# Kernel optimization log

Hardware: AMD Instinct MI355X
Metric: run time of the kernel (lower is better)

The kernel has to match this reference:

```python
import jax, jax.numpy as jnp
import numpy as np

# Config matching init_kwargs: layer_nb=1 -> stride 16, image 608x608 -> 38x38 grid
B, CIN, H, W = 32, 512, 38, 38
NA, NC = 3, 80
STRIDE = 16.0
ANCHORS = np.array([[30.0, 61.0], [62.0, 45.0], [59.0, 119.0]], dtype=np.float32)


def setup_inputs() -> dict:
    key = jax.random.key(0)
    k1, k2, k3 = jax.random.split(key, 3)
    xin = jax.random.normal(k1, (B, CIN, H, W), dtype=jnp.float32)
    # 1x1 conv weight stored as (out_ch, in_ch); out_ch = NA*(NC+5) = 255
    conv_w = jax.random.normal(k2, (NA * (NC + 5), CIN), dtype=jnp.float32) * 0.02
    conv_b = jax.random.normal(k3, (NA * (NC + 5),), dtype=jnp.float32) * 0.01
    return {"xin": xin, "conv_w": conv_w, "conv_b": conv_b}


def reference(xin, conv_w, conv_b):
    # 1x1 conv == channel GEMM; fuse the NCHW->NHWC permute into the einsum
    fm = jnp.einsum('bchw,oc->bhwo', xin, conv_w) + conv_b  # [B,H,W,255]
    fm = fm.reshape(B, H, W, NA, NC + 5)
    tx, ty, tw, th = fm[..., 0], fm[..., 1], fm[..., 2], fm[..., 3]
    # grid offsets (precomputed via broadcasting instead of per-call numpy rebuild)
    x_off = jnp.arange(W, dtype=fm.dtype)[None, None, :, None]   # broadcast over B,H,NA
    y_off = jnp.arange(H, dtype=fm.dtype)[None, :, None, None]   # broadcast over B,W,NA
    anchors = jnp.asarray(ANCHORS, dtype=fm.dtype)               # [NA,2]
    bx = (jax.nn.sigmoid(tx) + x_off) * STRIDE
    by = (jax.nn.sigmoid(ty) + y_off) * STRIDE
    bw = jnp.exp(tw) * anchors[:, 0]
    bh = jnp.exp(th) * anchors[:, 1]
    boxes = jnp.stack([bx, by, bw, bh], axis=-1)                 # [B,H,W,NA,4]
    # concat decoded boxes with raw objectness + class logits -> [B,H,W,NA,85]
    return jnp.concatenate([boxes, fm[..., 4:]], axis=-1)
```

## Files before the change

kernel.cpp:

```cpp
#include <hip/hip_runtime.h>
#include <hip/hip_bf16.h>
#include <cstdint>
#include <cstddef>

#define CIN_K  512
#define WW_    38
#define BHW    1444
#define NOUT   255
#define MTOT   46208

#define BM     32
#define ROW_E  520
#define EP_DW  260

typedef __attribute__((ext_vector_type(8))) short  bf16x8;
typedef __attribute__((ext_vector_type(4))) float  floatx4;

static __device__ __forceinline__ unsigned f2bf(float f) {
    unsigned u = __builtin_bit_cast(unsigned, f);
    return (u + 0x7FFFu + ((u >> 16) & 1u)) >> 16;
}

static __device__ __forceinline__ unsigned pk2bf(float a, float b) {
    __hip_bfloat162 h = __float22bfloat162_rn(make_float2(a, b));
    unsigned r;
    __builtin_memcpy(&r, &h, 4);
    return r;
}

__global__ void conv_w_to_bf16(const float* __restrict__ cw,
                               unsigned short* __restrict__ wb) {
    int tg   = blockIdx.x * 256 + threadIdx.x;
    int base = tg * 8;
    int n    = base >> 9;
    unsigned rr[4] = {0u, 0u, 0u, 0u};
    if (n < NOUT) {
        float4 v0 = *(const float4*)(cw + base);
        float4 v1 = *(const float4*)(cw + base + 4);
        rr[0] = f2bf(v0.x) | (f2bf(v0.y) << 16);
        rr[1] = f2bf(v0.z) | (f2bf(v0.w) << 16);
        rr[2] = f2bf(v1.x) | (f2bf(v1.y) << 16);
        rr[3] = f2bf(v1.z) | (f2bf(v1.w) << 16);
    }
    *(uint4*)(wb + base) = *(uint4*)rr;
}

__global__ __launch_bounds__(256, 4)
void yolo_head(const float* __restrict__ xin,
               const unsigned short* __restrict__ wb,
               const float* __restrict__ cb,
               float* __restrict__ out)
{
    __shared__ unsigned smem[BM * (ROW_E / 2)];
    unsigned short* As = (unsigned short*)smem;

    const int t    = threadIdx.x;
    const int w    = t >> 6;
    const int lane = t & 63;
    const int l15  = lane & 15;
    const int q    = lane >> 4;

    const int orig = blockIdx.x;
    const int xcd  = orig & 7;
    const int rank = orig >> 3;
    const int wgid = (xcd < 4 ? xcd * 181 : 724 + (xcd - 4) * 180) + rank;
    const int m0   = wgid * BM;

    const int mq4 = (t & 7) * 4;
    const int kq4 = (t >> 3) * 4;
    const int m4  = m0 + mq4;
    const int bi  = m4 / BHW;
    const int hw  = m4 - bi * BHW;
    const float* pb0 = xin + (size_t)bi * (CIN_K * BHW) + hw;

    alignas(16) float vv[4][4][4];
#pragma unroll
    for (int it = 0; it < 4; ++it)
#pragma unroll
        for (int kk = 0; kk < 4; ++kk)
            *(float4*)&vv[it][kk][0] =
                *(const float4*)(pb0 + (size_t)(it * 128 + kq4 + kk) * BHW);
#pragma unroll
    for (int it = 0; it < 4; ++it)
#pragma unroll
        for (int r = 0; r < 4; ++r) {
            unsigned lo = pk2bf(vv[it][0][r], vv[it][1][r]);
            unsigned hi = pk2bf(vv[it][2][r], vv[it][3][r]);
            *(uint2*)(&As[(mq4 + r) * ROW_E + it * 128 + kq4]) = make_uint2(lo, hi);
        }

    floatx4 acc[2][4];
#pragma unroll
    for (int i = 0; i < 2; ++i)
#pragma unroll
        for (int j = 0; j < 4; ++j)
            acc[i][j] = (floatx4){0.f, 0.f, 0.f, 0.f};

    const unsigned short* pbw = wb + (size_t)(w * 64 + l15) * CIN_K + q * 8;

    __syncthreads();

#pragma unroll
    for (int kc = 0; kc < 16; ++kc) {
        bf16x8 bfr[4], af[2];
#pragma unroll
        for (int j = 0; j < 4; ++j) {
            uint4 bv = *(const uint4*)(pbw + (size_t)j * 16 * CIN_K + kc * 32);
            bfr[j] = __builtin_bit_cast(bf16x8, bv);
        }
#pragma unroll
        for (int i = 0; i < 2; ++i) {
            int4 av = *(const int4*)(&As[(i * 16 + l15) * ROW_E + kc * 32 + q * 8]);
            af[i] = __builtin_bit_cast(bf16x8, av);
        }
#pragma unroll
        for (int i = 0; i < 2; ++i)
#pragma unroll
            for (int j = 0; j < 4; ++j)
                acc[i][j] = __builtin_amdgcn_mfma_f32_16x16x32_bf16(
                                af[i], bfr[j], acc[i][j], 0, 0, 0);
    }

#pragma unroll
    for (int j = 0; j < 4; ++j) {
        int   n    = w * 64 + j * 16 + l15;
        int   nc   = n < NOUT ? n : NOUT - 1;
        int   ai   = nc / 85;
        int   ji   = nc - ai * 85;
        float bias = cb[nc];
        float aw   = (ai == 0) ? 30.f : (ai == 1) ? 62.f : 59.f;
        float ah   = (ai == 0) ? 61.f : (ai == 1) ? 45.f : 119.f;
#pragma unroll
        for (int i = 0; i < 2; ++i)
#pragma unroll
            for (int r = 0; r < 4; ++r) {
                int   md  = m0 + i * 16 + q * 4 + r;
                int   rem = md % BHW;
                int   hh  = rem / WW_;
                float v   = acc[i][j][r] + bias;
                float res;
                if (ji == 0)      res = (1.f / (1.f + __expf(-v)) + (float)(rem - hh * WW_)) * 16.f;
                else if (ji == 1) res = (1.f / (1.f + __expf(-v)) + (float)hh) * 16.f;
                else if (ji == 2) res = __expf(v) * aw;
                else if (ji == 3) res = __expf(v) * ah;
                else              res = v;
                acc[i][j][r] = res;
            }
    }

    __syncthreads();
    float* EP = (float*)smem;
#pragma unroll
    for (int i = 0; i < 2; ++i)
#pragma unroll
        for (int j = 0; j < 4; ++j)
#pragma unroll
            for (int r = 0; r < 4; ++r)
                EP[(i * 16 + q * 4 + r) * EP_DW + w * 64 + j * 16 + l15] =
                    acc[i][j][r];
    __syncthreads();

    {
        const float* EPb = (const float*)smem + (w * 8) * EP_DW;
        float*       ob  = out + (size_t)(m0 + w * 8) * NOUT;
#pragma unroll
        for (int s2 = 0; s2 < 8; ++s2) {
            int f4 = s2 * 64 + lane;
            if (f4 < 510) {
                int   f = f4 * 4;
                float vs[4];
#pragma unroll
                for (int e = 0; e < 4; ++e) {
                    int fe = f + e;
                    int mr = fe / NOUT;
                    int x  = fe - mr * NOUT;
                    vs[e]  = EPb[mr * EP_DW + x];
                }
                *(float4*)(ob + f) = make_float4(vs[0], vs[1], vs[2], vs[3]);
            }
        }
    }
}

extern "C" void kernel_launch(void* const* d_in, const int* in_sizes, int n_in,
                              void* d_out, int out_size, void* d_ws, size_t ws_size,
                              hipStream_t stream) {
    const float* xin = (const float*)d_in[0];
    const float* cw  = (const float*)d_in[1];
    const float* cb  = (const float*)d_in[2];
    float*       out = (float*)d_out;
    unsigned short* wb = (unsigned short*)d_ws;

    hipLaunchKernelGGL(conv_w_to_bf16, dim3(64), dim3(256), 0, stream, cw, wb);
    hipLaunchKernelGGL(yolo_head, dim3(MTOT / BM), dim3(256), 0, stream,
                       xin, wb, cb, out);
}
```

Baseline: 196.6 us.

## Load activations directly into MFMA fragments and double the M tile

Removes the LDS staging of the activation tile. Each lane now gathers its 8 K-values straight from global memory, strided by BHW, and converts them to bf16 inside the K loop. BM goes from 32 to 64 so each weight fragment load feeds twice as many MFMAs, with the grid remapping and the epilogue adjusted to two 32-row passes. The cost is scalar, strided, 4-byte global loads on the critical path instead of float4 loads, more accumulator registers, and lower occupancy.

```diff
diff --git a/kernel.cpp b/kernel.cpp
--- a/kernel.cpp
+++ b/kernel.cpp
@@ -9,8 +9,7 @@
 #define NOUT   255
 #define MTOT   46208
 
-#define BM     32
-#define ROW_E  520
+#define BM     64
 #define EP_DW  260
 
 typedef __attribute__((ext_vector_type(8))) short  bf16x8;
@@ -45,14 +44,13 @@
     *(uint4*)(wb + base) = *(uint4*)rr;
 }
 
-__global__ __launch_bounds__(256, 4)
+__global__ __launch_bounds__(256, 3)
 void yolo_head(const float* __restrict__ xin,
                const unsigned short* __restrict__ wb,
                const float* __restrict__ cb,
                float* __restrict__ out)
 {
-    __shared__ unsigned smem[BM * (ROW_E / 2)];
-    unsigned short* As = (unsigned short*)smem;
+    __shared__ unsigned smem[32 * EP_DW];
 
     const int t    = threadIdx.x;
     const int w    = t >> 6;
@@ -63,58 +61,49 @@
     const int orig = blockIdx.x;
     const int xcd  = orig & 7;
     const int rank = orig >> 3;
-    const int wgid = (xcd < 4 ? xcd * 181 : 724 + (xcd - 4) * 180) + rank;
+    const int wgid = (xcd < 2 ? xcd * 91 : 182 + (xcd - 2) * 90) + rank;
     const int m0   = wgid * BM;
 
-    const int mq4 = (t & 7) * 4;
-    const int kq4 = (t >> 3) * 4;
-    const int m4  = m0 + mq4;
-    const int bi  = m4 / BHW;
-    const int hw  = m4 - bi * BHW;
-    const float* pb0 = xin + (size_t)bi * (CIN_K * BHW) + hw;
+    const float* pa[4];
+#pragma unroll
+    for (int i = 0; i < 4; ++i) {
+        int m  = m0 + i * 16 + l15;
+        int bi = m / BHW;
+        int hw = m - bi * BHW;
+        pa[i] = xin + (size_t)bi * (CIN_K * BHW) + hw + (size_t)(q * 8) * BHW;
+    }
 
-    alignas(16) float vv[4][4][4];
+    floatx4 acc[4][4];
 #pragma unroll
-    for (int it = 0; it < 4; ++it)
-#pragma unroll
-        for (int kk = 0; kk < 4; ++kk)
-            *(float4*)&vv[it][kk][0] =
-                *(const float4*)(pb0 + (size_t)(it * 128 + kq4 + kk) * BHW);
-#pragma unroll
-    for (int it = 0; it < 4; ++it)
-#pragma unroll
-        for (int r = 0; r < 4; ++r) {
-            unsigned lo = pk2bf(vv[it][0][r], vv[it][1][r]);
-            unsigned hi = pk2bf(vv[it][2][r], vv[it][3][r]);
-            *(uint2*)(&As[(mq4 + r) * ROW_E + it * 128 + kq4]) = make_uint2(lo, hi);
-        }
-
-    floatx4 acc[2][4];
-#pragma unroll
-    for (int i = 0; i < 2; ++i)
+    for (int i = 0; i < 4; ++i)
 #pragma unroll
         for (int j = 0; j < 4; ++j)
             acc[i][j] = (floatx4){0.f, 0.f, 0.f, 0.f};
 
     const unsigned short* pbw = wb + (size_t)(w * 64 + l15) * CIN_K + q * 8;
 
-    __syncthreads();
-
 #pragma unroll
     for (int kc = 0; kc < 16; ++kc) {
-        bf16x8 bfr[4], af[2];
+        bf16x8 bfr[4], af[4];
 #pragma unroll
         for (int j = 0; j < 4; ++j) {
             uint4 bv = *(const uint4*)(pbw + (size_t)j * 16 * CIN_K + kc * 32);
             bfr[j] = __builtin_bit_cast(bf16x8, bv);
         }
 #pragma unroll
-        for (int i = 0; i < 2; ++i) {
-            int4 av = *(const int4*)(&As[(i * 16 + l15) * ROW_E + kc * 32 + q * 8]);
-            af[i] = __builtin_bit_cast(bf16x8, av);
+        for (int i = 0; i < 4; ++i) {
+            float a8[8];
+#pragma unroll
+            for (int u = 0; u < 8; ++u)
+                a8[u] = pa[i][(size_t)(kc * 32 + u) * BHW];
+            unsigned d[4];
+#pragma unroll
+            for (int e = 0; e < 4; ++e)
+                d[e] = pk2bf(a8[2 * e], a8[2 * e + 1]);
+            af[i] = __builtin_bit_cast(bf16x8, *(uint4*)d);
         }
 #pragma unroll
-        for (int i = 0; i < 2; ++i)
+        for (int i = 0; i < 4; ++i)
 #pragma unroll
             for (int j = 0; j < 4; ++j)
                 acc[i][j] = __builtin_amdgcn_mfma_f32_16x16x32_bf16(
@@ -131,7 +120,7 @@
         float aw   = (ai == 0) ? 30.f : (ai == 1) ? 62.f : 59.f;
         float ah   = (ai == 0) ? 61.f : (ai == 1) ? 45.f : 119.f;
 #pragma unroll
-        for (int i = 0; i < 2; ++i)
+        for (int i = 0; i < 4; ++i)
 #pragma unroll
             for (int r = 0; r < 4; ++r) {
                 int   md  = m0 + i * 16 + q * 4 + r;
@@ -148,21 +137,24 @@
             }
     }
 
-    __syncthreads();
     float* EP = (float*)smem;
 #pragma unroll
-    for (int i = 0; i < 2; ++i)
+    for (int p = 0; p < 2; ++p) {
+        __syncthreads();
 #pragma unroll
-        for (int j = 0; j < 4; ++j)
+        for (int i2 = 0; i2 < 2; ++i2) {
+            const int i = p * 2 + i2;
 #pragma unroll
-            for (int r = 0; r < 4; ++r)
-                EP[(i * 16 + q * 4 + r) * EP_DW + w * 64 + j * 16 + l15] =
-                    acc[i][j][r];
-    __syncthreads();
+            for (int j = 0; j < 4; ++j)
+#pragma unroll
+                for (int r = 0; r < 4; ++r)
+                    EP[(i2 * 16 + q * 4 + r) * EP_DW + w * 64 + j * 16 + l15] =
+                        acc[i][j][r];
+        }
+        __syncthreads();
 
-    {
         const float* EPb = (const float*)smem + (w * 8) * EP_DW;
-        float*       ob  = out + (size_t)(m0 + w * 8) * NOUT;
+        float*       ob  = out + (size_t)(m0 + p * 32 + w * 8) * NOUT;
 #pragma unroll
         for (int s2 = 0; s2 < 8; ++s2) {
             int f4 = s2 * 64 + lane;
```

Result: slower. 210.8 us (+7.2%).

## Double M tile to 64 rows with 8 waves and K-chunked LDS staging

Applied to the files above, without the earlier changes.

Raises the block tile from 32 to 64 output rows with 512 threads arranged as 2x4 waves, so each weight fragment fetched from global memory is reused across twice as many rows. The A tile is staged through LDS in two K halves of 256, which keeps shared memory the same size but adds an extra barrier and reload step. The epilogue writes out the two 32-row halves in turn through the shared buffer. The risk is lower occupancy from the larger blocks and less overlap, since the load of the second K half waits behind the barrier.

```diff
diff --git a/kernel.cpp b/kernel.cpp
--- a/kernel.cpp
+++ b/kernel.cpp
@@ -9,8 +9,9 @@
 #define NOUT   255
 #define MTOT   46208
 
-#define BM     32
-#define ROW_E  520
+#define BM     64
+#define KCH    256
+#define ROW_E  260
 #define EP_DW  260
 
 typedef __attribute__((ext_vector_type(8))) short  bf16x8;
@@ -45,7 +46,7 @@
     *(uint4*)(wb + base) = *(uint4*)rr;
 }
 
-__global__ __launch_bounds__(256, 4)
+__global__ __launch_bounds__(512, 6)
 void yolo_head(const float* __restrict__ xin,
                const unsigned short* __restrict__ wb,
                const float* __restrict__ cb,
@@ -55,7 +56,9 @@
     unsigned short* As = (unsigned short*)smem;
 
     const int t    = threadIdx.x;
-    const int w    = t >> 6;
+    const int wv   = t >> 6;
+    const int wm   = wv >> 2;
+    const int wn   = wv & 3;
     const int lane = t & 63;
     const int l15  = lane & 15;
     const int q    = lane >> 4;
@@ -63,32 +66,16 @@
     const int orig = blockIdx.x;
     const int xcd  = orig & 7;
     const int rank = orig >> 3;
-    const int wgid = (xcd < 4 ? xcd * 181 : 724 + (xcd - 4) * 180) + rank;
+    const int wgid = (xcd < 2 ? xcd * 91 : 182 + (xcd - 2) * 90) + rank;
     const int m0   = wgid * BM;
 
-    const int mq4 = (t & 7) * 4;
-    const int kq4 = (t >> 3) * 4;
+    const int mq4 = (t & 15) * 4;
+    const int kq4 = (t >> 4) * 4;
     const int m4  = m0 + mq4;
     const int bi  = m4 / BHW;
     const int hw  = m4 - bi * BHW;
     const float* pb0 = xin + (size_t)bi * (CIN_K * BHW) + hw;
 
-    alignas(16) float vv[4][4][4];
-#pragma unroll
-    for (int it = 0; it < 4; ++it)
-#pragma unroll
-        for (int kk = 0; kk < 4; ++kk)
-            *(float4*)&vv[it][kk][0] =
-                *(const float4*)(pb0 + (size_t)(it * 128 + kq4 + kk) * BHW);
-#pragma unroll
-    for (int it = 0; it < 4; ++it)
-#pragma unroll
-        for (int r = 0; r < 4; ++r) {
-            unsigned lo = pk2bf(vv[it][0][r], vv[it][1][r]);
-            unsigned hi = pk2bf(vv[it][2][r], vv[it][3][r]);
-            *(uint2*)(&As[(mq4 + r) * ROW_E + it * 128 + kq4]) = make_uint2(lo, hi);
-        }
-
     floatx4 acc[2][4];
 #pragma unroll
     for (int i = 0; i < 2; ++i)
@@ -96,34 +83,59 @@
         for (int j = 0; j < 4; ++j)
             acc[i][j] = (floatx4){0.f, 0.f, 0.f, 0.f};
 
-    const unsigned short* pbw = wb + (size_t)(w * 64 + l15) * CIN_K + q * 8;
-
-    __syncthreads();
-
-#pragma unroll
-    for (int kc = 0; kc < 16; ++kc) {
-        bf16x8 bfr[4], af[2];
-#pragma unroll
-        for (int j = 0; j < 4; ++j) {
-            uint4 bv = *(const uint4*)(pbw + (size_t)j * 16 * CIN_K + kc * 32);
-            bfr[j] = __builtin_bit_cast(bf16x8, bv);
-        }
-#pragma unroll
-        for (int i = 0; i < 2; ++i) {
-            int4 av = *(const int4*)(&As[(i * 16 + l15) * ROW_E + kc * 32 + q * 8]);
-            af[i] = __builtin_bit_cast(bf16x8, av);
-        }
-#pragma unroll
-        for (int i = 0; i < 2; ++i)
-#pragma unroll
-            for (int j = 0; j < 4; ++j)
-                acc[i][j] = __builtin_amdgcn_mfma_f32_16x16x32_bf16(
-                                af[i], bfr[j], acc[i][j], 0, 0, 0);
+    const unsigned short* pbw = wb + (size_t)(wn * 64 + l15) * CIN_K + q * 8;
+
+#pragma unroll
+    for (int ck = 0; ck < 2; ++ck) {
+        if (ck) __syncthreads();
+
+        {
+            alignas(16) float vv[2][4][4];
+#pragma unroll
+            for (int s = 0; s < 2; ++s)
+#pragma unroll
+                for (int kk = 0; kk < 4; ++kk)
+                    *(float4*)&vv[s][kk][0] =
+                        *(const float4*)(pb0 + (size_t)(ck * KCH + s * 128 + kq4 + kk) * BHW);
+#pragma unroll
+            for (int s = 0; s < 2; ++s)
+#pragma unroll
+                for (int r = 0; r < 4; ++r) {
+                    unsigned lo = pk2bf(vv[s][0][r], vv[s][1][r]);
+                    unsigned hi = pk2bf(vv[s][2][r], vv[s][3][r]);
+                    *(uint2*)(&As[(mq4 + r) * ROW_E + s * 128 + kq4]) =
+                        make_uint2(lo, hi);
+                }
+        }
+        __syncthreads();
+
+#pragma unroll
+        for (int kc = 0; kc < 8; ++kc) {
+            bf16x8 bfr[4], af[2];
+#pragma unroll
+            for (int j = 0; j < 4; ++j) {
+                uint4 bv = *(const uint4*)(pbw + (size_t)j * 16 * CIN_K
+                                           + ck * KCH + kc * 32);
+                bfr[j] = __builtin_bit_cast(bf16x8, bv);
+            }
+#pragma unroll
+            for (int i = 0; i < 2; ++i) {
+                int4 av = *(const int4*)(&As[(wm * 32 + i * 16 + l15) * ROW_E
+                                             + kc * 32 + q * 8]);
+                af[i] = __builtin_bit_cast(bf16x8, av);
+            }
+#pragma unroll
+            for (int i = 0; i < 2; ++i)
+#pragma unroll
+                for (int j = 0; j < 4; ++j)
+                    acc[i][j] = __builtin_amdgcn_mfma_f32_16x16x32_bf16(
+                                    af[i], bfr[j], acc[i][j], 0, 0, 0);
+        }
     }
 
 #pragma unroll
     for (int j = 0; j < 4; ++j) {
-        int   n    = w * 64 + j * 16 + l15;
+        int   n    = wn * 64 + j * 16 + l15;
         int   nc   = n < NOUT ? n : NOUT - 1;
         int   ai   = nc / 85;
         int   ji   = nc - ai * 85;
@@ -134,7 +146,7 @@
         for (int i = 0; i < 2; ++i)
 #pragma unroll
             for (int r = 0; r < 4; ++r) {
-                int   md  = m0 + i * 16 + q * 4 + r;
+                int   md  = m0 + wm * 32 + i * 16 + q * 4 + r;
                 int   rem = md % BHW;
                 int   hh  = rem / WW_;
                 float v   = acc[i][j][r] + bias;
@@ -148,25 +160,27 @@
             }
     }
 
-    __syncthreads();
     float* EP = (float*)smem;
 #pragma unroll
-    for (int i = 0; i < 2; ++i)
-#pragma unroll
-        for (int j = 0; j < 4; ++j)
-#pragma unroll
-            for (int r = 0; r < 4; ++r)
-                EP[(i * 16 + q * 4 + r) * EP_DW + w * 64 + j * 16 + l15] =
-                    acc[i][j][r];
-    __syncthreads();
-
-    {
-        const float* EPb = (const float*)smem + (w * 8) * EP_DW;
-        float*       ob  = out + (size_t)(m0 + w * 8) * NOUT;
-#pragma unroll
-        for (int s2 = 0; s2 < 8; ++s2) {
-            int f4 = s2 * 64 + lane;
-            if (f4 < 510) {
+    for (int p = 0; p < 2; ++p) {
+        __syncthreads();
+        if (wm == p) {
+#pragma unroll
+            for (int i = 0; i < 2; ++i)
+#pragma unroll
+                for (int j = 0; j < 4; ++j)
+#pragma unroll
+                    for (int r = 0; r < 4; ++r)
+                        EP[(i * 16 + q * 4 + r) * EP_DW + wn * 64 + j * 16 + l15] =
+                            acc[i][j][r];
+        }
+        __syncthreads();
+
+        float* ob = out + (size_t)(m0 + p * 32) * NOUT;
+#pragma unroll
+        for (int s2 = 0; s2 < 4; ++s2) {
+            int f4 = s2 * 512 + t;
+            if (f4 < 2040) {
                 int   f = f4 * 4;
                 float vs[4];
 #pragma unroll
@@ -174,7 +188,7 @@
                     int fe = f + e;
                     int mr = fe / NOUT;
                     int x  = fe - mr * NOUT;
-                    vs[e]  = EPb[mr * EP_DW + x];
+                    vs[e]  = EP[mr * EP_DW + x];
                 }
                 *(float4*)(ob + f) = make_float4(vs[0], vs[1], vs[2], vs[3]);
             }
@@ -192,6 +206,6 @@
     unsigned short* wb = (unsigned short*)d_ws;
 
     hipLaunchKernelGGL(conv_w_to_bf16, dim3(64), dim3(256), 0, stream, cw, wb);
-    hipLaunchKernelGGL(yolo_head, dim3(MTOT / BM), dim3(256), 0, stream,
+    hipLaunchKernelGGL(yolo_head, dim3(MTOT / BM), dim3(512), 0, stream,
                        xin, wb, cb, out);
 }
```

Result: slower. 204.5 us (+4.0%).
